# Optimization experiments

Hardware: AMD Instinct MI355X
Metric: run time of the kernel (lower is better)

The kernel has to match this reference:

```python
import jax, jax.numpy as jnp
import numpy as np

B, L, H = 32, 256, 384
MAX_WAVE = 2048  # config.max_wave_length


def setup_inputs() -> dict:
    key = jax.random.key(0)
    k1, k2 = jax.random.split(key)
    encoder_hidden_states = jax.random.normal(k1, (B, L, H), dtype=jnp.float32)
    durations_gt = jax.random.randint(k2, (B, L), 0, 15, dtype=jnp.int32)
    return {"encoder_hidden_states": encoder_hidden_states, "durations_gt": durations_gt}


def reference(encoder_hidden_states, durations_gt):
    # Length regulation: token i is repeated durations_gt[b, i] times along the
    # output frame axis; frames past the total length are zero-padded.
    csum = jnp.cumsum(durations_gt, axis=1)               # [B, L] inclusive cumsum
    total = csum[:, -1]                                    # [B] real lengths
    t = jnp.arange(MAX_WAVE, dtype=csum.dtype)             # [T]
    # frame t belongs to token idx where csum[idx-1] <= t < csum[idx]
    idx = jax.vmap(lambda c: jnp.searchsorted(c, t, side="right"))(csum)  # [B, T]
    valid = t[None, :] < total[:, None]                    # [B, T]
    safe_idx = jnp.clip(idx, 0, L - 1)
    gathered = jnp.take_along_axis(encoder_hidden_states, safe_idx[..., None], axis=1)  # [B, T, H]
    gathered = jnp.where(valid[..., None], gathered, 0.0)
    outputs = jnp.transpose(gathered, (0, 2, 1))           # [B, H, T] per custom-op output shape
    encoder_masks = valid.astype(encoder_hidden_states.dtype)  # [B, T]
    return outputs, encoder_masks
```

## Files before the change

### kernel.cpp

```cpp
#include <hip/hip_runtime.h>

constexpr int Lc = 256;
constexpr int Hc = 384;
constexpr int Tc = 2048;
constexpr int Bc = 32;
constexpr int H_TILE = 16;

typedef float floatx4 __attribute__((ext_vector_type(4)));

__global__ __launch_bounds__(512) void lr_fused_kernel(
    const float* __restrict__ enc,
    const int*   __restrict__ dur,
    float*       __restrict__ out,
    float*       __restrict__ mask)
{
    const int tid  = threadIdx.x;
    const int lane = tid & 63;
    const int wv   = tid >> 6;
    const int b    = blockIdx.y;
    const int h0   = blockIdx.x * H_TILE;

    __shared__ unsigned short s_row[Tc];
    __shared__ int            s_wtot[8];

    int d = 0;
    if (tid < Lc) d = dur[b * Lc + tid];
    {
        uint2 f; f.x = 0x00FF00FFu; f.y = 0x00FF00FFu;
        *reinterpret_cast<uint2*>(s_row + tid * 4) = f;
    }

    int s = d;
#pragma unroll
    for (int off = 1; off < 64; off <<= 1) {
        int t = __shfl_up(s, off);
        if (lane >= off) s += t;
    }
    if (lane == 63) s_wtot[wv] = s;

    __syncthreads();

    int pre = 0, total = 0;
#pragma unroll
    for (int w = 0; w < 4; ++w) {
        int t = s_wtot[w];
        total += t;
        if (w < wv) pre += t;
    }
    if (tid < Lc) {
        const int csum_i = s + pre;
        const int excl   = csum_i - d;
        int hiw = csum_i; if (hiw > Tc) hiw = Tc;
        for (int t = excl; t < hiw; ++t) s_row[t] = (unsigned short)tid;
    }

    __syncthreads();

    const int tbase = tid * 4;
    ushort4 iv = *reinterpret_cast<const ushort4*>(s_row + tbase);

    const float* encb = enc + (size_t)b * (Lc * Hc) + h0;
    const float* rp0 = encb + (size_t)iv.x * Hc;
    const float* rp1 = encb + (size_t)iv.y * Hc;
    const float* rp2 = encb + (size_t)iv.z * Hc;
    const float* rp3 = encb + (size_t)iv.w * Hc;

    const float m0 = (tbase + 0 < total) ? 1.0f : 0.0f;
    const float m1 = (tbase + 1 < total) ? 1.0f : 0.0f;
    const float m2 = (tbase + 2 < total) ? 1.0f : 0.0f;
    const float m3 = (tbase + 3 < total) ? 1.0f : 0.0f;

    float* outb = out + (size_t)b * (Hc * Tc) + (size_t)h0 * Tc + tbase;
#pragma unroll
    for (int hh0 = 0; hh0 < H_TILE; hh0 += 4) {
        floatx4 a0 = *reinterpret_cast<const floatx4*>(rp0 + hh0);
        floatx4 a1 = *reinterpret_cast<const floatx4*>(rp1 + hh0);
        floatx4 a2 = *reinterpret_cast<const floatx4*>(rp2 + hh0);
        floatx4 a3 = *reinterpret_cast<const floatx4*>(rp3 + hh0);
#pragma unroll
        for (int j = 0; j < 4; ++j) {
            floatx4 v;
            v.x = a0[j] * m0;
            v.y = a1[j] * m1;
            v.z = a2[j] * m2;
            v.w = a3[j] * m3;
            *reinterpret_cast<floatx4*>(outb + (size_t)(hh0 + j) * Tc) = v;
        }
    }

    if (blockIdx.x == 0) {
        floatx4 m; m.x = m0; m.y = m1; m.z = m2; m.w = m3;
        *reinterpret_cast<floatx4*>(mask + (size_t)b * Tc + tbase) = m;
    }
}

extern "C" void kernel_launch(void* const* d_in, const int* in_sizes, int n_in,
                              void* d_out, int out_size, void* d_ws, size_t ws_size,
                              hipStream_t stream) {
    const float* enc = (const float*)d_in[0];
    const int*   dur = (const int*)d_in[1];

    float* out  = (float*)d_out;
    float* mask = out + (size_t)Bc * Hc * Tc;

    dim3 grid(Hc / H_TILE, Bc);
    dim3 block(512);
    lr_fused_kernel<<<grid, block, 0, stream>>>(enc, dur, out, mask);
}
```

Before: 26.40 us.

## Stage encoder tile in padded LDS and gather from shared memory per wave

The encoder slice for the block (256 tokens by 16 hidden) is loaded coalesced into padded shared memory up front, overlapping the duration scan. The output loop is restructured so each wave handles one hidden row at a time over all frames, gathering from LDS instead of scattered global loads. Output and mask writes use nontemporal stores. This removes uncoalesced global gathers but adds LDS traffic, scalar LDS reads and higher shared-memory use, which may lower occupancy.

```diff
diff --git a/kernel.cpp b/kernel.cpp
--- a/kernel.cpp
+++ b/kernel.cpp
@@ -5,6 +5,7 @@
 constexpr int Tc = 2048;
 constexpr int Bc = 32;
 constexpr int H_TILE = 16;
+constexpr int PADW = 17;
 
 typedef float floatx4 __attribute__((ext_vector_type(4)));
 
@@ -20,8 +21,15 @@
     const int b    = blockIdx.y;
     const int h0   = blockIdx.x * H_TILE;
 
+    __shared__ float          s_enc[Lc * PADW];
     __shared__ unsigned short s_row[Tc];
     __shared__ int            s_wtot[8];
+
+    const float* encb = enc + (size_t)b * (Lc * Hc) + h0;
+    const int r  = tid >> 2;
+    const int c4 = (tid & 3) * 4;
+    floatx4 st0 = *reinterpret_cast<const floatx4*>(encb + (size_t)r * Hc + c4);
+    floatx4 st1 = *reinterpret_cast<const floatx4*>(encb + (size_t)(r + 128) * Hc + c4);
 
     int d = 0;
     if (tid < Lc) d = dur[b * Lc + tid];
@@ -37,6 +45,13 @@
         if (lane >= off) s += t;
     }
     if (lane == 63) s_wtot[wv] = s;
+
+    {
+        float* d0 = s_enc + r * PADW + c4;
+        d0[0] = st0.x; d0[1] = st0.y; d0[2] = st0.z; d0[3] = st0.w;
+        float* d1 = s_enc + (r + 128) * PADW + c4;
+        d1[0] = st1.x; d1[1] = st1.y; d1[2] = st1.z; d1[3] = st1.w;
+    }
 
     __syncthreads();
 
@@ -56,41 +71,37 @@
 
     __syncthreads();
 
-    const int tbase = tid * 4;
-    ushort4 iv = *reinterpret_cast<const ushort4*>(s_row + tbase);
+    ushort4 ivv[8];
+#pragma unroll
+    for (int it = 0; it < 8; ++it)
+        ivv[it] = *reinterpret_cast<const ushort4*>(s_row + it * 256 + lane * 4);
 
-    const float* encb = enc + (size_t)b * (Lc * Hc) + h0;
-    const float* rp0 = encb + (size_t)iv.x * Hc;
-    const float* rp1 = encb + (size_t)iv.y * Hc;
-    const float* rp2 = encb + (size_t)iv.z * Hc;
-    const float* rp3 = encb + (size_t)iv.w * Hc;
-
-    const float m0 = (tbase + 0 < total) ? 1.0f : 0.0f;
-    const float m1 = (tbase + 1 < total) ? 1.0f : 0.0f;
-    const float m2 = (tbase + 2 < total) ? 1.0f : 0.0f;
-    const float m3 = (tbase + 3 < total) ? 1.0f : 0.0f;
-
-    float* outb = out + (size_t)b * (Hc * Tc) + (size_t)h0 * Tc + tbase;
+    float* outB = out + (size_t)b * (Hc * Tc) + (size_t)h0 * Tc;
 #pragma unroll
-    for (int hh0 = 0; hh0 < H_TILE; hh0 += 4) {
-        floatx4 a0 = *reinterpret_cast<const floatx4*>(rp0 + hh0);
-        floatx4 a1 = *reinterpret_cast<const floatx4*>(rp1 + hh0);
-        floatx4 a2 = *reinterpret_cast<const floatx4*>(rp2 + hh0);
-        floatx4 a3 = *reinterpret_cast<const floatx4*>(rp3 + hh0);
+    for (int hp = 0; hp < 2; ++hp) {
+        const int h = wv + hp * 8;
+        float* outrow = outB + (size_t)h * Tc;
 #pragma unroll
-        for (int j = 0; j < 4; ++j) {
+        for (int it = 0; it < 8; ++it) {
+            const int t0 = it * 256 + lane * 4;
             floatx4 v;
-            v.x = a0[j] * m0;
-            v.y = a1[j] * m1;
-            v.z = a2[j] * m2;
-            v.w = a3[j] * m3;
-            *reinterpret_cast<floatx4*>(outb + (size_t)(hh0 + j) * Tc) = v;
+            v.x = s_enc[(int)ivv[it].x * PADW + h] * ((t0 + 0 < total) ? 1.0f : 0.0f);
+            v.y = s_enc[(int)ivv[it].y * PADW + h] * ((t0 + 1 < total) ? 1.0f : 0.0f);
+            v.z = s_enc[(int)ivv[it].z * PADW + h] * ((t0 + 2 < total) ? 1.0f : 0.0f);
+            v.w = s_enc[(int)ivv[it].w * PADW + h] * ((t0 + 3 < total) ? 1.0f : 0.0f);
+            __builtin_nontemporal_store(v, reinterpret_cast<floatx4*>(outrow + t0));
         }
     }
 
     if (blockIdx.x == 0) {
-        floatx4 m; m.x = m0; m.y = m1; m.z = m2; m.w = m3;
-        *reinterpret_cast<floatx4*>(mask + (size_t)b * Tc + tbase) = m;
+        const int tb = tid * 4;
+        floatx4 m;
+        m.x = (tb + 0 < total) ? 1.0f : 0.0f;
+        m.y = (tb + 1 < total) ? 1.0f : 0.0f;
+        m.z = (tb + 2 < total) ? 1.0f : 0.0f;
+        m.w = (tb + 3 < total) ? 1.0f : 0.0f;
+        __builtin_nontemporal_store(
+            m, reinterpret_cast<floatx4*>(mask + (size_t)b * Tc + tb));
     }
 }
 
```

Result: faster. 24.40 us (-7.6%).
